# Kernel optimization log

Measured on AMD Instinct MI355X. Metric: run time of the kernel, lower is better.

The kernel has to match this reference:

```python
import jax, jax.numpy as jnp
import numpy as np

NEG_BIG = -9e15
ALPHA = 0.2  # LeakyReLU negative slope


def setup_inputs() -> dict:
    key = jax.random.key(0)
    k1, k2, k3, k4 = jax.random.split(key, 4)
    N, Fin, Fout = 8192, 256, 256
    input_ = jax.random.normal(k1, (N, Fin), dtype=jnp.float32)
    adj = jax.random.randint(k2, (N, N), 0, 2, dtype=jnp.int32)
    # xavier_uniform with gain=1.414
    limW = 1.414 * np.sqrt(6.0 / (Fin + Fout))
    W = jax.random.uniform(k3, (Fin, Fout), minval=-limW, maxval=limW, dtype=jnp.float32)
    lima = 1.414 * np.sqrt(6.0 / (2 * Fout + 1))
    a = jax.random.uniform(k4, (2 * Fout, 1), minval=-lima, maxval=lima, dtype=jnp.float32)
    return {"input_": input_, "adj": adj, "W": W, "a": a}


def reference(input_, adj, W, a):
    # h: [N, F]
    h = input_ @ W
    F = h.shape[1]
    # Decompose cat([h_i, h_j]) @ a into per-node projections summed by broadcast
    src = h @ a[:F, 0]   # [N]  contribution of row node i
    dst = h @ a[F:, 0]   # [N]  contribution of col node j
    e = jax.nn.leaky_relu(src[:, None] + dst[None, :], negative_slope=ALPHA)  # [N, N]
    e = jnp.where(adj > 0, e, NEG_BIG)
    attention = jax.nn.softmax(e, axis=1)
    h_prime = attention @ h  # [N, F]
    return jax.nn.relu(h_prime)  # concat=True
```

## Files before the change

### kernel.cpp

```cpp
#include <hip/hip_runtime.h>
#include <math.h>

#define NN 8192
#define FF 256
#define ALPHA 0.2f

typedef __bf16 bf16x8 __attribute__((ext_vector_type(8)));
typedef __bf16 bf16x4 __attribute__((ext_vector_type(4)));
typedef float  f32x4  __attribute__((ext_vector_type(4)));

__device__ __forceinline__ void dma16(const void* g, void* l) {
    __builtin_amdgcn_global_load_lds((const __attribute__((address_space(1))) void*)g,
                                     (__attribute__((address_space(3))) void*)l,
                                     16, 0, 0);
}

#define VMCNT3   asm volatile("s_waitcnt vmcnt(3)" ::: "memory")
#define LGKM0    asm volatile("s_waitcnt lgkmcnt(0)" ::: "memory")
#define BARRIER  asm volatile("s_barrier" ::: "memory")
#define FENCE    asm volatile("" ::: "memory")

__global__ __launch_bounds__(256) void k0_wt(const float* __restrict__ W,
                                             __bf16* __restrict__ WT) {
    __shared__ float ts[64][65];
    const int t = threadIdx.x;
    const int k0 = blockIdx.x * 64;
    const int n0 = blockIdx.y * 64;
    #pragma unroll
    for (int r = 0; r < 4; ++r) {
        int krow = r * 16 + (t >> 4);
        int nc4 = (t & 15) * 4;
        *(float4*)&ts[krow][nc4] = *(const float4*)&W[(size_t)(k0 + krow) * FF + n0 + nc4];
    }
    __syncthreads();
    const int nloc = t >> 2;
    const int kc = (t & 3) * 16;
    union { bf16x8 v[2]; __bf16 e[16]; } hi, lo;
    #pragma unroll
    for (int u = 0; u < 16; ++u) {
        float x = ts[kc + u][nloc];
        __bf16 h1 = (__bf16)x;
        hi.e[u] = h1;
        lo.e[u] = (__bf16)(x - (float)h1);
    }
    size_t base = (size_t)(n0 + nloc) * FF + k0 + kc;
    *(bf16x8*)&WT[base] = hi.v[0];
    *(bf16x8*)&WT[base + 8] = hi.v[1];
    size_t lbase = (size_t)FF * FF + base;
    *(bf16x8*)&WT[lbase] = lo.v[0];
    *(bf16x8*)&WT[lbase + 8] = lo.v[1];
}

__global__ __launch_bounds__(256) void k5_pack(const int* __restrict__ adj,
                                               unsigned int* __restrict__ mask) {
    const int wv = threadIdx.x >> 6, l = threadIdx.x & 63;
    const size_t nwords = (size_t)NN * NN / 64;
    const size_t nw = (size_t)gridDim.x * 4;
    for (size_t w = (size_t)blockIdx.x * 4 + wv; w < nwords; w += nw) {
        int v = adj[w * 64 + l];
        unsigned long long b = __ballot(v > 0);
        if (l == 0) *(unsigned long long*)&mask[w * 2] = b;
    }
}

__global__ __launch_bounds__(256) void k1_h(const float* __restrict__ X,
                                            const __bf16* __restrict__ WT,
                                            const float* __restrict__ a,
                                            __bf16* __restrict__ hT,
                                            float* __restrict__ src,
                                            float* __restrict__ dst) {
    __shared__ __bf16 ax[2][32][40];
    __shared__ float hs[32][264];
    __shared__ float red[2][4][32];
    const int t = threadIdx.x;
    const int i0 = blockIdx.x * 32;
    const int l = t & 63, wv = t >> 6, ln = l & 15, g = l >> 4;
    f32x4 acc[2][4];
    #pragma unroll
    for (int mt = 0; mt < 2; ++mt)
        #pragma unroll
        for (int nt = 0; nt < 4; ++nt)
            acc[mt][nt] = (f32x4){0.f, 0.f, 0.f, 0.f};

    for (int ks = 0; ks < 8; ++ks) {
        const int k0 = ks * 32;
        {
            int row = t >> 3, c4 = (t & 7) * 4;
            float4 xv = *(const float4*)&X[(size_t)(i0 + row) * FF + k0 + c4];
            bf16x4 hi4, lo4;
            float xs_[4] = {xv.x, xv.y, xv.z, xv.w};
            #pragma unroll
            for (int u = 0; u < 4; ++u) {
                __bf16 h1 = (__bf16)xs_[u];
                hi4[u] = h1;
                lo4[u] = (__bf16)(xs_[u] - (float)h1);
            }
            *(bf16x4*)&ax[0][row][c4] = hi4;
            *(bf16x4*)&ax[1][row][c4] = lo4;
        }
        __syncthreads();
        bf16x8 ah[2], al[2];
        ah[0] = *(bf16x8*)&ax[0][ln][g * 8];
        ah[1] = *(bf16x8*)&ax[0][16 + ln][g * 8];
        al[0] = *(bf16x8*)&ax[1][ln][g * 8];
        al[1] = *(bf16x8*)&ax[1][16 + ln][g * 8];
        #pragma unroll
        for (int nt = 0; nt < 4; ++nt) {
            const int n = wv * 64 + nt * 16 + ln;
            bf16x8 bh8 = *(const bf16x8*)&WT[(size_t)n * FF + k0 + g * 8];
            bf16x8 bl8 = *(const bf16x8*)&WT[(size_t)(FF + n) * FF + k0 + g * 8];
            #pragma unroll
            for (int mt = 0; mt < 2; ++mt) {
                acc[mt][nt] = __builtin_amdgcn_mfma_f32_16x16x32_bf16(ah[mt], bh8, acc[mt][nt], 0, 0, 0);
                acc[mt][nt] = __builtin_amdgcn_mfma_f32_16x16x32_bf16(ah[mt], bl8, acc[mt][nt], 0, 0, 0);
                acc[mt][nt] = __builtin_amdgcn_mfma_f32_16x16x32_bf16(al[mt], bh8, acc[mt][nt], 0, 0, 0);
            }
        }
        __syncthreads();
    }
    float an[4], ad[4];
    #pragma unroll
    for (int nt = 0; nt < 4; ++nt) {
        an[nt] = a[wv * 64 + nt * 16 + ln];
        ad[nt] = a[FF + wv * 64 + nt * 16 + ln];
    }
    float sp[2][4], dp[2][4];
    #pragma unroll
    for (int mt = 0; mt < 2; ++mt)
        #pragma unroll
        for (int rg = 0; rg < 4; ++rg) { sp[mt][rg] = 0.f; dp[mt][rg] = 0.f; }
    #pragma unroll
    for (int mt = 0; mt < 2; ++mt)
        #pragma unroll
        for (int nt = 0; nt < 4; ++nt)
            #pragma unroll
            for (int rg = 0; rg < 4; ++rg) {
                float v = acc[mt][nt][rg];
                hs[mt * 16 + g * 4 + rg][wv * 64 + nt * 16 + ln] = v;
                sp[mt][rg] += v * an[nt];
                dp[mt][rg] += v * ad[nt];
            }
    #pragma unroll
    for (int mk = 1; mk < 16; mk <<= 1)
        #pragma unroll
        for (int mt = 0; mt < 2; ++mt)
            #pragma unroll
            for (int rg = 0; rg < 4; ++rg) {
                sp[mt][rg] += __shfl_xor(sp[mt][rg], mk);
                dp[mt][rg] += __shfl_xor(dp[mt][rg], mk);
            }
    if (ln == 0) {
        #pragma unroll
        for (int mt = 0; mt < 2; ++mt)
            #pragma unroll
            for (int rg = 0; rg < 4; ++rg) {
                red[0][wv][mt * 16 + g * 4 + rg] = sp[mt][rg];
                red[1][wv][mt * 16 + g * 4 + rg] = dp[mt][rg];
            }
    }
    __syncthreads();
    if (t < 32) {
        src[i0 + t] = red[0][0][t] + red[0][1][t] + red[0][2][t] + red[0][3][t];
        dst[i0 + t] = red[1][0][t] + red[1][1][t] + red[1][2][t] + red[1][3][t];
    }
    {
        const int f = t;
        #pragma unroll
        for (int jc = 0; jc < 4; ++jc) {
            union { bf16x8 v; __bf16 e[8]; } hi;
            #pragma unroll
            for (int u = 0; u < 8; ++u)
                hi.e[u] = (__bf16)hs[jc * 8 + u][f];
            *(bf16x8*)&hT[(size_t)f * NN + i0 + jc * 8] = hi.v;
        }
    }
}

__global__ __launch_bounds__(256) void k2b_max(const float* __restrict__ dst,
                                               float* __restrict__ maxd) {
    __shared__ float red[256];
    float m = -1e30f;
    #pragma unroll
    for (int r = 0; r < NN / 1024; ++r) {
        float4 v = *(const float4*)&dst[(r * 256 + threadIdx.x) * 4];
        m = fmaxf(m, fmaxf(fmaxf(v.x, v.y), fmaxf(v.z, v.w)));
    }
    red[threadIdx.x] = m;
    __syncthreads();
    for (int s = 128; s > 0; s >>= 1) {
        if (threadIdx.x < s) red[threadIdx.x] = fmaxf(red[threadIdx.x], red[threadIdx.x + s]);
        __syncthreads();
    }
    if (threadIdx.x == 0) maxd[0] = red[0];
}

__global__ __launch_bounds__(256, 4) void k3_attn(const unsigned int* __restrict__ mask,
                                                  const __bf16* __restrict__ hT,
                                                  const float* __restrict__ src,
                                                  const float* __restrict__ dst,
                                                  const float* __restrict__ maxd,
                                                  float* __restrict__ num,
                                                  float* __restrict__ den,
                                                  int jseg, int steps) {
    __shared__ __bf16 bh[2][1024 * 8];
    const int t = threadIdx.x;
    const int l = t & 63, wv = t >> 6, ln = l & 15, g = l >> 4;
    const int it = blockIdx.x & 127;
    const int seg = blockIdx.x >> 7;
    const int i0 = it * 64;
    const int jbeg = seg * jseg;
    const int row = i0 + wv * 16 + ln;
    const float maxdv = maxd[0];
    const float src_r = src[row];
    const float e0 = src_r + maxdv;
    const float m_r = e0 > 0.f ? e0 : ALPHA * e0;

    int ga[4], cb[4];
    #pragma unroll
    for (int r = 0; r < 4; ++r) {
        int cbase = r * 256 + wv * 64;
        int c = cbase + l;
        int f = c >> 2;
        int pc = c & 3;
        int jc = pc ^ ((f >> 1) & 3);
        ga[r] = f * NN + jc * 8;
        cb[r] = __builtin_amdgcn_readfirstlane(cbase);
    }
    const unsigned int* mrow = mask + (size_t)row * (NN / 32) + (jbeg >> 5);
    const float* drow = dst + g * 8;

    const int rb = ln * 64 + ((g ^ ((ln >> 1) & 3)) * 16);
    const char* bh0 = (const char*)&bh[0][0] + rb;
    const char* bh1 = (const char*)&bh[1][0] + rb;

    unsigned int mE, mO;
    float4 d0e, d1e, d0o, d1o;

    mE = mrow[0];
    d0e = *(const float4*)(drow + jbeg);
    d1e = *(const float4*)(drow + jbeg + 4);
    FENCE;
    #pragma unroll
    for (int r = 0; r < 4; ++r)
        dma16(&hT[ga[r] + jbeg], &bh[0][cb[r] * 8]);
    FENCE;
    mO = mrow[1];
    d0o = *(const float4*)(drow + jbeg + 32);
    d1o = *(const float4*)(drow + jbeg + 32 + 4);
    FENCE;

    float den_reg = 0.f;
    f32x4 acc[16];
    #pragma unroll
    for (int nt = 0; nt < 16; ++nt) acc[nt] = (f32x4){0.f, 0.f, 0.f, 0.f};

#define K3_WCOMP(M_, D0_, D1_, AF_)                                           \
    {                                                                         \
        const unsigned int bits = ((M_) >> (g * 8)) & 0xffu;                  \
        const float dv[8] = {D0_.x, D0_.y, D0_.z, D0_.w,                      \
                             D1_.x, D1_.y, D1_.z, D1_.w};                     \
        _Pragma("unroll")                                                     \
        for (int u = 0; u < 8; ++u) {                                         \
            float e = src_r + dv[u];                                          \
            e = e > 0.f ? e : ALPHA * e;                                      \
            float w = ((bits >> u) & 1u) ? __expf(e - m_r) : 0.f;             \
            den_reg += w;                                                     \
            AF_[u] = (__bf16)w;                                               \
        }                                                                     \
    }

#define K3_PREF(M_, D0_, D1_, SN_)                                            \
    M_ = mrow[SN_];                                                           \
    D0_ = *(const float4*)(drow + jbeg + (SN_) * 32);                         \
    D1_ = *(const float4*)(drow + jbeg + (SN_) * 32 + 4);

#define K3_DMA(J1_, P_)                                                       \
    {                                                                         \
        _Pragma("unroll")                                                     \
        for (int r = 0; r < 4; ++r)                                           \
            dma16(&hT[ga[r] + (J1_)], &bh[P_][cb[r] * 8]);                    \
    }

#define K3_MFMA(AF_, BP_)                                                     \
    {                                                                         \
        _Pragma("unroll")                                                     \
        for (int nt = 0; nt < 16; ++nt) {                                     \
            bf16x8 bfr = *(const bf16x8*)((BP_) + nt * 1024);                 \
            acc[nt] = __builtin_amdgcn_mfma_f32_16x16x32_bf16(                \
                AF_, bfr, acc[nt], 0, 0, 0);                                  \
        }                                                                     \
    }

    for (int su = 0; su < steps; su += 2) {
        bf16x8 afe;
        K3_WCOMP(mE, d0e, d1e, afe);
        {
            const int sn = (su + 2 < steps) ? su + 2 : 0;
            K3_PREF(mE, d0e, d1e, sn);
        }
        FENCE; VMCNT3; LGKM0; BARRIER;
        K3_DMA(jbeg + (su + 1) * 32, 1);
        FENCE;
        K3_MFMA(afe, bh0);
        bf16x8 afo;
        K3_WCOMP(mO, d0o, d1o, afo);
        {
            const int sn = (su + 3 < steps) ? su + 3 : 0;
            K3_PREF(mO, d0o, d1o, sn);
        }
        FENCE; VMCNT3; LGKM0; BARRIER;
        {
            const int s2 = (su + 2 < steps) ? su + 2 : 0;
            K3_DMA(jbeg + s2 * 32, 0);
        }
        FENCE;
        K3_MFMA(afo, bh1);
    }
    den_reg += __shfl_xor(den_reg, 16);
    den_reg += __shfl_xor(den_reg, 32);
    if (g == 0) den[(size_t)seg * NN + row] = den_reg;
    #pragma unroll
    for (int nt = 0; nt < 16; ++nt)
        #pragma unroll
        for (int rg = 0; rg < 4; ++rg)
            num[((size_t)seg * NN + i0 + wv * 16 + g * 4 + rg) * FF
                + nt * 16 + ln] = acc[nt][rg];
}

__global__ __launch_bounds__(256) void k4_out(const float* __restrict__ num,
                                              const float* __restrict__ den,
                                              float* __restrict__ out, int S) {
    size_t f4 = (size_t)blockIdx.x * 256 + threadIdx.x;
    int i = (int)(f4 >> 6);
    int c4 = (int)(f4 & 63) << 2;
    float4 s = make_float4(0.f, 0.f, 0.f, 0.f);
    float d = 0.f;
    for (int sg = 0; sg < S; ++sg) {
        float4 v = *(const float4*)&num[((size_t)sg * NN + i) * FF + c4];
        s.x += v.x; s.y += v.y; s.z += v.z; s.w += v.w;
        d += den[(size_t)sg * NN + i];
    }
    float inv = 1.f / d;
    float4 o;
    o.x = fmaxf(s.x * inv, 0.f);
    o.y = fmaxf(s.y * inv, 0.f);
    o.z = fmaxf(s.z * inv, 0.f);
    o.w = fmaxf(s.w * inv, 0.f);
    *(float4*)&out[(size_t)i * FF + c4] = o;
}

extern "C" void kernel_launch(void* const* d_in, const int* in_sizes, int n_in,
                              void* d_out, int out_size, void* d_ws, size_t ws_size,
                              hipStream_t stream) {
    const float* X  = (const float*)d_in[0];
    const int*  adj = (const int*)d_in[1];
    const float* W  = (const float*)d_in[2];
    const float* a  = (const float*)d_in[3];
    float* out = (float*)d_out;
    char* ws = (char*)d_ws;

    const size_t off_hT   = 0;
    const size_t off_mask = off_hT + (size_t)NN * FF * 2;
    const size_t off_wt   = off_mask + (size_t)NN * (NN / 32) * 4;
    const size_t off_src  = off_wt + (size_t)2 * FF * FF * 2;
    const size_t off_dst  = off_src + (size_t)NN * 4;
    const size_t off_maxd = off_dst + (size_t)NN * 4;
    const size_t off_num  = off_maxd + 256;

    int SSv = 8;
    if (off_num + (size_t)8 * NN * FF * 4 + (size_t)8 * NN * 4 > ws_size) SSv = 4;
    const size_t off_den = off_num + (size_t)SSv * NN * FF * 4;
    const int jseg = NN / SSv;
    const int steps = jseg / 32;

    __bf16* hT_ws = (__bf16*)(ws + off_hT);
    unsigned int* mask_ws = (unsigned int*)(ws + off_mask);
    __bf16* wt_ws = (__bf16*)(ws + off_wt);
    float* src_ws = (float*)(ws + off_src);
    float* dst_ws = (float*)(ws + off_dst);
    float* maxd   = (float*)(ws + off_maxd);
    float* num_ws = (float*)(ws + off_num);
    float* den_ws = (float*)(ws + off_den);

    k5_pack<<<2048, 256, 0, stream>>>(adj, mask_ws);
    k0_wt<<<dim3(FF / 64, FF / 64), 256, 0, stream>>>(W, wt_ws);
    k1_h<<<NN / 32, 256, 0, stream>>>(X, wt_ws, a, hT_ws, src_ws, dst_ws);
    k2b_max<<<1, 256, 0, stream>>>(dst_ws, maxd);
    k3_attn<<<128 * SSv, 256, 0, stream>>>(mask_ws, hT_ws, src_ws, dst_ws, maxd,
                                           num_ws, den_ws, jseg, steps);
    k4_out<<<(NN * FF / 4) / 256, 256, 0, stream>>>(num_ws, den_ws, out, SSv);
}
```

Baseline: 475.2 us.

## Split attention tile so each wave computes two row groups over half the features

Each wave in the attention kernel previously handled 16 rows across all 256 feature columns. Now it handles two 16-row groups across half of the feature columns. Each LDS B-fragment read then feeds two MFMAs, halving LDS read traffic per MFMA. The cost is that exp/weight computation is duplicated across the two feature-half waves, and there are more mask loads per wave. The vmcnt wait threshold and the occupancy hint in launch bounds are adjusted to match the extra loads and register use.

```diff
diff --git a/kernel.cpp b/kernel.cpp
--- a/kernel.cpp
+++ b/kernel.cpp
@@ -15,7 +15,7 @@
                                      16, 0, 0);
 }
 
-#define VMCNT3   asm volatile("s_waitcnt vmcnt(3)" ::: "memory")
+#define VMCNT4   asm volatile("s_waitcnt vmcnt(4)" ::: "memory")
 #define LGKM0    asm volatile("s_waitcnt lgkmcnt(0)" ::: "memory")
 #define BARRIER  asm volatile("s_barrier" ::: "memory")
 #define FENCE    asm volatile("" ::: "memory")
@@ -194,7 +194,7 @@
     if (threadIdx.x == 0) maxd[0] = red[0];
 }
 
-__global__ __launch_bounds__(256, 4) void k3_attn(const unsigned int* __restrict__ mask,
+__global__ __launch_bounds__(256, 3) void k3_attn(const unsigned int* __restrict__ mask,
                                                   const __bf16* __restrict__ hT,
                                                   const float* __restrict__ src,
                                                   const float* __restrict__ dst,
@@ -205,15 +205,18 @@
     __shared__ __bf16 bh[2][1024 * 8];
     const int t = threadIdx.x;
     const int l = t & 63, wv = t >> 6, ln = l & 15, g = l >> 4;
+    const int rgp = wv >> 1, fh = wv & 1;
     const int it = blockIdx.x & 127;
     const int seg = blockIdx.x >> 7;
     const int i0 = it * 64;
     const int jbeg = seg * jseg;
-    const int row = i0 + wv * 16 + ln;
+    const int rowA = i0 + rgp * 32 + ln;
+    const int rowB = rowA + 16;
     const float maxdv = maxd[0];
-    const float src_r = src[row];
-    const float e0 = src_r + maxdv;
-    const float m_r = e0 > 0.f ? e0 : ALPHA * e0;
+    const float srcA = src[rowA], srcB = src[rowB];
+    const float eA0 = srcA + maxdv, eB0 = srcB + maxdv;
+    const float mA_ = eA0 > 0.f ? eA0 : ALPHA * eA0;
+    const float mB_ = eB0 > 0.f ? eB0 : ALPHA * eB0;
 
     int ga[4], cb[4];
     #pragma unroll
@@ -226,17 +229,19 @@
         ga[r] = f * NN + jc * 8;
         cb[r] = __builtin_amdgcn_readfirstlane(cbase);
     }
-    const unsigned int* mrow = mask + (size_t)row * (NN / 32) + (jbeg >> 5);
+    const unsigned int* mrowA = mask + (size_t)rowA * (NN / 32) + (jbeg >> 5);
+    const unsigned int* mrowB = mask + (size_t)rowB * (NN / 32) + (jbeg >> 5);
     const float* drow = dst + g * 8;
 
-    const int rb = ln * 64 + ((g ^ ((ln >> 1) & 3)) * 16);
+    const int rb = fh * 8192 + ln * 64 + ((g ^ ((ln >> 1) & 3)) * 16);
     const char* bh0 = (const char*)&bh[0][0] + rb;
     const char* bh1 = (const char*)&bh[1][0] + rb;
 
-    unsigned int mE, mO;
+    unsigned int mAe, mBe, mAo, mBo;
     float4 d0e, d1e, d0o, d1o;
 
-    mE = mrow[0];
+    mAe = mrowA[0];
+    mBe = mrowB[0];
     d0e = *(const float4*)(drow + jbeg);
     d1e = *(const float4*)(drow + jbeg + 4);
     FENCE;
@@ -244,33 +249,44 @@
     for (int r = 0; r < 4; ++r)
         dma16(&hT[ga[r] + jbeg], &bh[0][cb[r] * 8]);
     FENCE;
-    mO = mrow[1];
+    mAo = mrowA[1];
+    mBo = mrowB[1];
     d0o = *(const float4*)(drow + jbeg + 32);
     d1o = *(const float4*)(drow + jbeg + 32 + 4);
     FENCE;
 
-    float den_reg = 0.f;
-    f32x4 acc[16];
-    #pragma unroll
-    for (int nt = 0; nt < 16; ++nt) acc[nt] = (f32x4){0.f, 0.f, 0.f, 0.f};
-
-#define K3_WCOMP(M_, D0_, D1_, AF_)                                           \
+    float denA = 0.f, denB = 0.f;
+    f32x4 accA[8], accB[8];
+    #pragma unroll
+    for (int nt = 0; nt < 8; ++nt) {
+        accA[nt] = (f32x4){0.f, 0.f, 0.f, 0.f};
+        accB[nt] = (f32x4){0.f, 0.f, 0.f, 0.f};
+    }
+
+#define K3_WCOMP(MA_, MB_, D0_, D1_, AFA_, AFB_)                              \
     {                                                                         \
-        const unsigned int bits = ((M_) >> (g * 8)) & 0xffu;                  \
+        const unsigned int ba = ((MA_) >> (g * 8)) & 0xffu;                   \
+        const unsigned int bb = ((MB_) >> (g * 8)) & 0xffu;                   \
         const float dv[8] = {D0_.x, D0_.y, D0_.z, D0_.w,                      \
                              D1_.x, D1_.y, D1_.z, D1_.w};                     \
         _Pragma("unroll")                                                     \
         for (int u = 0; u < 8; ++u) {                                         \
-            float e = src_r + dv[u];                                          \
-            e = e > 0.f ? e : ALPHA * e;                                      \
-            float w = ((bits >> u) & 1u) ? __expf(e - m_r) : 0.f;             \
-            den_reg += w;                                                     \
-            AF_[u] = (__bf16)w;                                               \
+            float eA = srcA + dv[u];                                          \
+            eA = eA > 0.f ? eA : ALPHA * eA;                                  \
+            float wA = ((ba >> u) & 1u) ? __expf(eA - mA_) : 0.f;             \
+            denA += wA;                                                       \
+            AFA_[u] = (__bf16)wA;                                             \
+            float eB = srcB + dv[u];                                          \
+            eB = eB > 0.f ? eB : ALPHA * eB;                                  \
+            float wB = ((bb >> u) & 1u) ? __expf(eB - mB_) : 0.f;             \
+            denB += wB;                                                       \
+            AFB_[u] = (__bf16)wB;                                             \
         }                                                                     \
     }
 
-#define K3_PREF(M_, D0_, D1_, SN_)                                            \
-    M_ = mrow[SN_];                                                           \
+#define K3_PREF(MA_, MB_, D0_, D1_, SN_)                                      \
+    MA_ = mrowA[SN_];                                                         \
+    MB_ = mrowB[SN_];                                                         \
     D0_ = *(const float4*)(drow + jbeg + (SN_) * 32);                         \
     D1_ = *(const float4*)(drow + jbeg + (SN_) * 32 + 4);
 
@@ -281,50 +297,59 @@
             dma16(&hT[ga[r] + (J1_)], &bh[P_][cb[r] * 8]);                    \
     }
 
-#define K3_MFMA(AF_, BP_)                                                     \
+#define K3_MFMA(AFA_, AFB_, BP_)                                              \
     {                                                                         \
         _Pragma("unroll")                                                     \
-        for (int nt = 0; nt < 16; ++nt) {                                     \
+        for (int nt = 0; nt < 8; ++nt) {                                      \
             bf16x8 bfr = *(const bf16x8*)((BP_) + nt * 1024);                 \
-            acc[nt] = __builtin_amdgcn_mfma_f32_16x16x32_bf16(                \
-                AF_, bfr, acc[nt], 0, 0, 0);                                  \
+            accA[nt] = __builtin_amdgcn_mfma_f32_16x16x32_bf16(               \
+                AFA_, bfr, accA[nt], 0, 0, 0);                                \
+            accB[nt] = __builtin_amdgcn_mfma_f32_16x16x32_bf16(               \
+                AFB_, bfr, accB[nt], 0, 0, 0);                                \
         }                                                                     \
     }
 
     for (int su = 0; su < steps; su += 2) {
-        bf16x8 afe;
-        K3_WCOMP(mE, d0e, d1e, afe);
+        bf16x8 afA, afB;
+        K3_WCOMP(mAe, mBe, d0e, d1e, afA, afB);
         {
             const int sn = (su + 2 < steps) ? su + 2 : 0;
-            K3_PREF(mE, d0e, d1e, sn);
-        }
-        FENCE; VMCNT3; LGKM0; BARRIER;
+            K3_PREF(mAe, mBe, d0e, d1e, sn);
+        }
+        FENCE; VMCNT4; LGKM0; BARRIER;
         K3_DMA(jbeg + (su + 1) * 32, 1);
         FENCE;
-        K3_MFMA(afe, bh0);
-        bf16x8 afo;
-        K3_WCOMP(mO, d0o, d1o, afo);
+        K3_MFMA(afA, afB, bh0);
+        bf16x8 afC, afD;
+        K3_WCOMP(mAo, mBo, d0o, d1o, afC, afD);
         {
             const int sn = (su + 3 < steps) ? su + 3 : 0;
-            K3_PREF(mO, d0o, d1o, sn);
-        }
-        FENCE; VMCNT3; LGKM0; BARRIER;
+            K3_PREF(mAo, mBo, d0o, d1o, sn);
+        }
+        FENCE; VMCNT4; LGKM0; BARRIER;
         {
             const int s2 = (su + 2 < steps) ? su + 2 : 0;
             K3_DMA(jbeg + s2 * 32, 0);
         }
         FENCE;
-        K3_MFMA(afo, bh1);
-    }
-    den_reg += __shfl_xor(den_reg, 16);
-    den_reg += __shfl_xor(den_reg, 32);
-    if (g == 0) den[(size_t)seg * NN + row] = den_reg;
-    #pragma unroll
-    for (int nt = 0; nt < 16; ++nt)
-        #pragma unroll
-        for (int rg = 0; rg < 4; ++rg)
-            num[((size_t)seg * NN + i0 + wv * 16 + g * 4 + rg) * FF
-                + nt * 16 + ln] = acc[nt][rg];
+        K3_MFMA(afC, afD, bh1);
+    }
+    denA += __shfl_xor(denA, 16);
+    denA += __shfl_xor(denA, 32);
+    denB += __shfl_xor(denB, 16);
+    denB += __shfl_xor(denB, 32);
+    if (g == 0 && fh == 0) {
+        den[(size_t)seg * NN + rowA] = denA;
+        den[(size_t)seg * NN + rowB] = denB;
+    }
+    #pragma unroll
+    for (int nt = 0; nt < 8; ++nt)
+        #pragma unroll
+        for (int rg = 0; rg < 4; ++rg) {
+            const int fcol = fh * 128 + nt * 16 + ln;
+            num[((size_t)seg * NN + i0 + rgp * 32 + g * 4 + rg) * FF + fcol] = accA[nt][rg];
+            num[((size_t)seg * NN + i0 + rgp * 32 + 16 + g * 4 + rg) * FF + fcol] = accB[nt][rg];
+        }
 }
 
 __global__ __launch_bounds__(256) void k4_out(const float* __restrict__ num,
```

Result: slower. 500.5 us (+5.3%).

## Pair warps to share attention weights via LDS and halve B-fragment reads

Applied to the files above, without the earlier changes.

Warps now work in pairs. Each warp still computes the masked softmax weights for its own 16 rows, then publishes them to a small double-buffered LDS area so its partner can read them. Each warp then accumulates 32 rows by 128 features instead of 16 rows by 256, so each B fragment read from LDS feeds two MFMAs. This halves LDS traffic for the hT tile, at the cost of an extra LDS write and read of the weight fragments per step and reliance on the existing barriers for ordering.

```diff
diff --git a/kernel.cpp b/kernel.cpp
--- a/kernel.cpp
+++ b/kernel.cpp
@@ -203,15 +203,17 @@
                                                   float* __restrict__ den,
                                                   int jseg, int steps) {
     __shared__ __bf16 bh[2][1024 * 8];
+    __shared__ __bf16 wsh[2][2][2][512];
     const int t = threadIdx.x;
     const int l = t & 63, wv = t >> 6, ln = l & 15, g = l >> 4;
+    const int rgp = wv >> 1, fh = wv & 1;
     const int it = blockIdx.x & 127;
     const int seg = blockIdx.x >> 7;
     const int i0 = it * 64;
     const int jbeg = seg * jseg;
-    const int row = i0 + wv * 16 + ln;
+    const int rowO = i0 + rgp * 32 + fh * 16 + ln;
     const float maxdv = maxd[0];
-    const float src_r = src[row];
+    const float src_r = src[rowO];
     const float e0 = src_r + maxdv;
     const float m_r = e0 > 0.f ? e0 : ALPHA * e0;
 
@@ -226,12 +228,16 @@
         ga[r] = f * NN + jc * 8;
         cb[r] = __builtin_amdgcn_readfirstlane(cbase);
     }
-    const unsigned int* mrow = mask + (size_t)row * (NN / 32) + (jbeg >> 5);
+    const unsigned int* mrow = mask + (size_t)rowO * (NN / 32) + (jbeg >> 5);
     const float* drow = dst + g * 8;
 
-    const int rb = ln * 64 + ((g ^ ((ln >> 1) & 3)) * 16);
+    const int rb = fh * 8192 + ln * 64 + ((g ^ ((ln >> 1) & 3)) * 16);
     const char* bh0 = (const char*)&bh[0][0] + rb;
     const char* bh1 = (const char*)&bh[1][0] + rb;
+    __bf16* wshW0 = &wsh[0][rgp][fh][l * 8];
+    __bf16* wshW1 = &wsh[1][rgp][fh][l * 8];
+    const __bf16* wshR0 = &wsh[0][rgp][fh ^ 1][l * 8];
+    const __bf16* wshR1 = &wsh[1][rgp][fh ^ 1][l * 8];
 
     unsigned int mE, mO;
     float4 d0e, d1e, d0o, d1o;
@@ -250,9 +256,12 @@
     FENCE;
 
     float den_reg = 0.f;
-    f32x4 acc[16];
-    #pragma unroll
-    for (int nt = 0; nt < 16; ++nt) acc[nt] = (f32x4){0.f, 0.f, 0.f, 0.f};
+    f32x4 accO[8], accP[8];
+    #pragma unroll
+    for (int nt = 0; nt < 8; ++nt) {
+        accO[nt] = (f32x4){0.f, 0.f, 0.f, 0.f};
+        accP[nt] = (f32x4){0.f, 0.f, 0.f, 0.f};
+    }
 
 #define K3_WCOMP(M_, D0_, D1_, AF_)                                           \
     {                                                                         \
@@ -281,50 +290,62 @@
             dma16(&hT[ga[r] + (J1_)], &bh[P_][cb[r] * 8]);                    \
     }
 
-#define K3_MFMA(AF_, BP_)                                                     \
+#define K3_MFMA(AFO_, AFP_, BP_)                                              \
     {                                                                         \
         _Pragma("unroll")                                                     \
-        for (int nt = 0; nt < 16; ++nt) {                                     \
+        for (int nt = 0; nt < 8; ++nt) {                                      \
             bf16x8 bfr = *(const bf16x8*)((BP_) + nt * 1024);                 \
-            acc[nt] = __builtin_amdgcn_mfma_f32_16x16x32_bf16(                \
-                AF_, bfr, acc[nt], 0, 0, 0);                                  \
+            accO[nt] = __builtin_amdgcn_mfma_f32_16x16x32_bf16(               \
+                AFO_, bfr, accO[nt], 0, 0, 0);                                \
+            accP[nt] = __builtin_amdgcn_mfma_f32_16x16x32_bf16(               \
+                AFP_, bfr, accP[nt], 0, 0, 0);                                \
         }                                                                     \
     }
 
     for (int su = 0; su < steps; su += 2) {
-        bf16x8 afe;
-        K3_WCOMP(mE, d0e, d1e, afe);
         {
-            const int sn = (su + 2 < steps) ? su + 2 : 0;
-            K3_PREF(mE, d0e, d1e, sn);
-        }
-        FENCE; VMCNT3; LGKM0; BARRIER;
-        K3_DMA(jbeg + (su + 1) * 32, 1);
-        FENCE;
-        K3_MFMA(afe, bh0);
-        bf16x8 afo;
-        K3_WCOMP(mO, d0o, d1o, afo);
+            bf16x8 afO;
+            K3_WCOMP(mE, d0e, d1e, afO);
+            *(bf16x8*)wshW0 = afO;
+            {
+                const int sn = (su + 2 < steps) ? su + 2 : 0;
+                K3_PREF(mE, d0e, d1e, sn);
+            }
+            FENCE; VMCNT3; LGKM0; BARRIER;
+            K3_DMA(jbeg + (su + 1) * 32, 1);
+            FENCE;
+            bf16x8 afP = *(const bf16x8*)wshR0;
+            K3_MFMA(afO, afP, bh0);
+        }
         {
-            const int sn = (su + 3 < steps) ? su + 3 : 0;
-            K3_PREF(mO, d0o, d1o, sn);
-        }
-        FENCE; VMCNT3; LGKM0; BARRIER;
-        {
-            const int s2 = (su + 2 < steps) ? su + 2 : 0;
-            K3_DMA(jbeg + s2 * 32, 0);
-        }
-        FENCE;
-        K3_MFMA(afo, bh1);
+            bf16x8 afO;
+            K3_WCOMP(mO, d0o, d1o, afO);
+            *(bf16x8*)wshW1 = afO;
+            {
+                const int sn = (su + 3 < steps) ? su + 3 : 0;
+                K3_PREF(mO, d0o, d1o, sn);
+            }
+            FENCE; VMCNT3; LGKM0; BARRIER;
+            {
+                const int s2 = (su + 2 < steps) ? su + 2 : 0;
+                K3_DMA(jbeg + s2 * 32, 0);
+            }
+            FENCE;
+            bf16x8 afP = *(const bf16x8*)wshR1;
+            K3_MFMA(afO, afP, bh1);
+        }
     }
     den_reg += __shfl_xor(den_reg, 16);
     den_reg += __shfl_xor(den_reg, 32);
-    if (g == 0) den[(size_t)seg * NN + row] = den_reg;
-    #pragma unroll
-    for (int nt = 0; nt < 16; ++nt)
-        #pragma unroll
-        for (int rg = 0; rg < 4; ++rg)
-            num[((size_t)seg * NN + i0 + wv * 16 + g * 4 + rg) * FF
-                + nt * 16 + ln] = acc[nt][rg];
+    if (g == 0) den[(size_t)seg * NN + rowO] = den_reg;
+    #pragma unroll
+    for (int nt = 0; nt < 8; ++nt)
+        #pragma unroll
+        for (int rg = 0; rg < 4; ++rg) {
+            const int fcol = fh * 128 + nt * 16 + ln;
+            num[((size_t)seg * NN + i0 + rgp * 32 + fh * 16 + g * 4 + rg) * FF + fcol] = accO[nt][rg];
+            num[((size_t)seg * NN + i0 + rgp * 32 + (fh ^ 1) * 16 + g * 4 + rg) * FF + fcol] = accP[nt][rg];
+        }
 }
 
 __global__ __launch_bounds__(256) void k4_out(const float* __restrict__ num,
```

Result: no change. 469.2 us (-1.3%).
